# Optimization experiments

Hardware: AMD Instinct MI355X
Metric: run time of the kernel (lower is better)

## Reference

```python
import jax, jax.numpy as jnp
import numpy as np

B, D, S = 16384, 1024, 1024

def _layernorm(x, g, b, eps=1e-5):
    mu = jnp.mean(x, axis=-1, keepdims=True)
    var = jnp.mean(jnp.square(x - mu), axis=-1, keepdims=True)
    return (x - mu) * jax.lax.rsqrt(var + eps) * g + b

def setup_inputs() -> dict:
    key = jax.random.key(0)
    ks = jax.random.split(key, 8)
    inv = lambda n: 1.0 / np.sqrt(n)
    return {
        "x": jax.random.normal(ks[0], (B, D), jnp.float32),
        "s_prev0": jax.random.normal(ks[1], (B, S), jnp.float32),
        "s_prev1": jax.random.normal(ks[2], (B, S), jnp.float32),
        "Wi": jax.random.uniform(ks[3], (4 * S, D), jnp.float32, -inv(D), inv(D)),
        "Ws": jax.random.uniform(ks[4], (4 * S, 2 * S), jnp.float32, -inv(2 * S), inv(2 * S)),
        "lni_g": jnp.ones((4 * S,), jnp.float32),
        "lni_b": jnp.zeros((4 * S,), jnp.float32),
        "lns_g": jnp.ones((4 * S,), jnp.float32),
        "lns_b": jnp.zeros((4 * S,), jnp.float32),
        "lnh_g": jnp.ones((S,), jnp.float32),
        "lnh_b": jnp.zeros((S,), jnp.float32),
    }

def reference(x, s_prev0, s_prev1, Wi, Ws, lni_g, lni_b, lns_g, lns_b, lnh_g, lnh_b):
    s = jnp.concatenate([s_prev0, s_prev1], axis=-1)  # [B, 2S]
    igates = _layernorm(x @ Wi.T, lni_g, lni_b)        # [B, 4S]
    sgates = _layernorm(s @ Ws.T, lns_g, lns_b)        # [B, 4S]
    gates = igates + sgates
    r_inv, i, n, l = jnp.split(gates, 4, axis=1)
    s_n = sgates[:, 2 * S:3 * S]
    l = jax.nn.sigmoid(l)
    r_inv = jax.nn.sigmoid(r_inv)
    i = jax.nn.sigmoid(i)
    n = jnp.tanh(n - r_inv * s_n)
    h = n + i * (l * s_prev0 + (1.0 - l) * s_prev1 - n)
    return _layernorm(h, lnh_g, lnh_b)
```

## Files before the change

### kernel.cpp

```cpp
#include <hip/hip_runtime.h>
#include <cstdint>


typedef unsigned short ushort_t;
typedef __attribute__((ext_vector_type(8))) __bf16 bf16x8;
typedef __attribute__((ext_vector_type(4))) float f32x4;

__device__ __forceinline__ ushort_t f2b(float f) {
    unsigned u = __float_as_uint(f);
    unsigned r = (u + 0x7fffu + ((u >> 16) & 1u)) >> 16;
    return (ushort_t)r;
}
__device__ __forceinline__ float b2f(ushort_t u) {
    return __uint_as_float(((unsigned)u) << 16);
}

__device__ __forceinline__ void gl_lds16(const void* g, void* l) {
    __builtin_amdgcn_global_load_lds(
        (const __attribute__((address_space(1))) unsigned int*)(uintptr_t)g,
        (__attribute__((address_space(3))) unsigned int*)(uintptr_t)l,
        16, 0, 0);
}

#define LOG2E 1.4426950408889634f
__device__ __forceinline__ float fexp2(float x) { return __builtin_amdgcn_exp2f(x); }
__device__ __forceinline__ float frcp(float x)  { return __builtin_amdgcn_rcpf(x); }
__device__ __forceinline__ float fsigmoid(float x) {
    return frcp(1.f + fexp2(-LOG2E * x));
}
__device__ __forceinline__ float ftanh(float y) {
    return 1.f - 2.f * frcp(1.f + fexp2((2.f * LOG2E) * y));
}

__global__ __launch_bounds__(256) void cast_bf16(const float* __restrict__ src,
                                                 ushort_t* __restrict__ dst, long n) {
    long i = ((long)blockIdx.x * 256 + threadIdx.x) * 4;
    if (i + 3 < n) {
        float4 v = *(const float4*)(src + i);
        ushort4 u;
        u.x = f2b(v.x); u.y = f2b(v.y); u.z = f2b(v.z); u.w = f2b(v.w);
        *(ushort4*)(dst + i) = u;
    }
}

__global__ __launch_bounds__(256) void cast_concat(const float* __restrict__ s0,
                                                   const float* __restrict__ s1,
                                                   ushort_t* __restrict__ dst) {
    long i = ((long)blockIdx.x * 256 + threadIdx.x) * 4;
    long row = i >> 11;
    int  col = (int)(i & 2047);
    const float* src = (col < 1024) ? (s0 + row * 1024 + col)
                                    : (s1 + row * 1024 + (col - 1024));
    float4 v = *(const float4*)src;
    ushort4 u;
    u.x = f2b(v.x); u.y = f2b(v.y); u.z = f2b(v.z); u.w = f2b(v.w);
    *(ushort4*)(dst + i) = u;
}


__device__ __forceinline__ void stage2(const char* s0, const char* s1,
                                       int d0, int d1, char* ldsbase,
                                       int kt, int NT) {
    if (kt < NT) {
        long kb = (long)kt << 7;
        char* lb = ldsbase + ((kt & 1) << 15);
        gl_lds16(s0 + kb, lb + d0);
        gl_lds16(s1 + kb, lb + d1);
    }
}

#define SGB_MFMA(n) __builtin_amdgcn_sched_group_barrier(0x8, n, 0)
#define SGB_DSR(n)  __builtin_amdgcn_sched_group_barrier(0x100, n, 0)

#define MFMA_II(Q, II, BS)                                                    \
    _Pragma("unroll") for (int jj = 0; jj < 2; jj++)                          \
        _Pragma("unroll") for (int kh = 0; kh < 2; kh++)                      \
            acc[Q][II][jj] = __builtin_amdgcn_mfma_f32_16x16x32_bf16(         \
                af[II][kh], bfr[BS][jj][kh], acc[Q][II][jj], 0, 0, 0);

#define MFMA_JJ(Q, JJ, BS)                                                    \
    _Pragma("unroll") for (int ii = 0; ii < 4; ii++)                          \
        _Pragma("unroll") for (int kh = 0; kh < 2; kh++)                      \
            acc[Q][ii][JJ] = __builtin_amdgcn_mfma_f32_16x16x32_bf16(         \
                af[ii][kh], bfr[BS][JJ][kh], acc[Q][ii][JJ], 0, 0, 0);

#define RD_B(BASE, R16, KC) (*(const bf16x8*)((BASE) + brow + (R16) * 2048 + (KC)))
#define RD_A(BASE, R16, KC) (*(const bf16x8*)((BASE) + arow + (R16) * 2048 + (KC)))

__global__ __launch_bounds__(512, 2) void gemm_bt(const ushort_t* __restrict__ A,
                                                  const ushort_t* __restrict__ W,
                                                  ushort_t* __restrict__ C,
                                                  int M, int N, int K) {
    (void)M;
    __shared__ __align__(16) ushort_t As[2][256 * 64];
    __shared__ __align__(16) ushort_t Bs[2][256 * 64];

    const int NT   = K >> 6;
    const int t    = threadIdx.x;
    const int lane = t & 63;
    const int w    = t >> 6;
    const int gm   = w >> 2;
    const int gn   = w & 3;
    const int gb   = gn & 1;
    const int wm   = gm << 7;
    const int wn   = gn << 6;

    const int nwg  = gridDim.x;
    const int cpx  = nwg >> 3;
    const int orig = blockIdx.x;
    const int wgid = (orig & 7) * cpx + (orig >> 3);
    const int NXB  = N >> 8;
    const int bx   = wgid % NXB;
    const int by   = wgid / NXB;
    const int bm0  = by << 8;
    const int bn0  = bx << 8;

    const int u0r = t >> 3;
    const int chb = (t & 7) << 4;
    const int cbs = chb ^ ((u0r & 7) << 4);
    const int ur0 = u0r, ur1 = 64 + u0r;

    #define AER(ur) ((ur) < 64 ? (ur) : (ur) + 128)
    #define ALR(ur) ((ur) + 64)
    #define BER(ur) (((((ur) >> 5) >> 1) << 7) + ((((ur) >> 5) & 1) * 96) + ((ur) & 31))
    #define BLR(ur) ((ur) + 32 + (((ur) >> 6) << 6))

    const char* sAe0 = (const char*)(A + (long)(bm0 + AER(ur0)) * K) + cbs;
    const char* sAe1 = (const char*)(A + (long)(bm0 + AER(ur1)) * K) + cbs;
    const char* sAl0 = (const char*)(A + (long)(bm0 + ALR(ur0)) * K) + cbs;
    const char* sAl1 = (const char*)(A + (long)(bm0 + ALR(ur1)) * K) + cbs;
    const char* sBe0 = (const char*)(W + (long)(bn0 + BER(ur0)) * K) + cbs;
    const char* sBe1 = (const char*)(W + (long)(bn0 + BER(ur1)) * K) + cbs;
    const char* sBl0 = (const char*)(W + (long)(bn0 + BLR(ur0)) * K) + cbs;
    const char* sBl1 = (const char*)(W + (long)(bn0 + BLR(ur1)) * K) + cbs;

    const int dAe0 = AER(ur0) * 128 + chb, dAe1 = AER(ur1) * 128 + chb;
    const int dAl0 = ALR(ur0) * 128 + chb, dAl1 = ALR(ur1) * 128 + chb;
    const int dBe0 = BER(ur0) * 128 + chb, dBe1 = BER(ur1) * 128 + chb;
    const int dBl0 = BLR(ur0) * 128 + chb, dBl1 = BLR(ur1) * 128 + chb;

    char* Abase = (char*)&As[0][0];
    char* Bbase = (char*)&Bs[0][0];

    const int ml   = lane & 15;
    const int g    = lane >> 4;
    const int rsw  = (lane & 7) << 4;
    const int kc0  = ((g << 4)) ^ rsw;
    const int kc1  = (64 | (g << 4)) ^ rsw;
    const int arow = (wm + ml) << 7;
    const int brow = (wn + ml) << 7;

    f32x4 acc[4][4][2];
#pragma unroll
    for (int q = 0; q < 4; q++)
#pragma unroll
        for (int ii = 0; ii < 4; ii++)
#pragma unroll
            for (int jj = 0; jj < 2; jj++)
                acc[q][ii][jj] = (f32x4){0.f, 0.f, 0.f, 0.f};

    bf16x8 af[4][2];
    bf16x8 bfr[2][2][2];

    stage2(sAe0, sAe1, dAe0, dAe1, Abase, 0, NT);
    stage2(sAl0, sAl1, dAl0, dAl1, Abase, 0, NT);
    stage2(sBe0, sBe1, dBe0, dBe1, Bbase, 0, NT);
    stage2(sBl0, sBl1, dBl0, dBl1, Bbase, 0, NT);
    stage2(sAe0, sAe1, dAe0, dAe1, Abase, 1, NT);
    stage2(sBe0, sBe1, dBe0, dBe1, Bbase, 1, NT);
    asm volatile("s_waitcnt vmcnt(4)" ::: "memory");
    __builtin_amdgcn_s_barrier();
#pragma unroll
    for (int jj = 0; jj < 2; jj++) {
        bfr[0][jj][0] = RD_B(Bbase, (gb << 1) + jj, kc0);
        bfr[0][jj][1] = RD_B(Bbase, (gb << 1) + jj, kc1);
    }
#pragma unroll
    for (int ii = 0; ii < 4; ii++) {
        af[ii][0] = RD_A(Abase, (gm << 2) + ii, kc0);
        af[ii][1] = RD_A(Abase, (gm << 2) + ii, kc1);
    }

    for (int kt = 0; kt < NT; ++kt) {
        const char* AbT = Abase + ((kt & 1) << 15);
        const char* BbT = Bbase + ((kt & 1) << 15);
        const char* AbN = Abase + (((kt + 1) & 1) << 15);
        const char* BbN = Bbase + (((kt + 1) & 1) << 15);
        const int rB1 = (1 ^ gb) << 1;
        const int rB0 = gb << 1;
        const int rA1 = (1 ^ gm) << 2;
        const int rA0 = gm << 2;

        stage2(sAl0, sAl1, dAl0, dAl1, Abase, kt + 1, NT);
        __builtin_amdgcn_s_barrier();
        __builtin_amdgcn_s_setprio(1);
        MFMA_II(0, 0, 0); SGB_MFMA(4);
        bfr[1][0][0] = RD_B(BbT, rB1 + 0, kc0); SGB_DSR(1);
        MFMA_II(0, 1, 0); SGB_MFMA(4);
        bfr[1][0][1] = RD_B(BbT, rB1 + 0, kc1); SGB_DSR(1);
        MFMA_II(0, 2, 0); SGB_MFMA(4);
        bfr[1][1][0] = RD_B(BbT, rB1 + 1, kc0); SGB_DSR(1);
        MFMA_II(0, 3, 0); SGB_MFMA(4);
        bfr[1][1][1] = RD_B(BbT, rB1 + 1, kc1); SGB_DSR(1);
        __builtin_amdgcn_s_setprio(0);

        stage2(sBl0, sBl1, dBl0, dBl1, Bbase, kt + 1, NT);
        __builtin_amdgcn_s_barrier();
        __builtin_amdgcn_s_setprio(1);
        MFMA_II(1, 0, 1); SGB_MFMA(4);
        af[0][0] = RD_A(AbT, rA1 + 0, kc0);
        af[0][1] = RD_A(AbT, rA1 + 0, kc1); SGB_DSR(2);
        MFMA_II(1, 1, 1); SGB_MFMA(4);
        af[1][0] = RD_A(AbT, rA1 + 1, kc0);
        af[1][1] = RD_A(AbT, rA1 + 1, kc1); SGB_DSR(2);
        MFMA_II(1, 2, 1); SGB_MFMA(4);
        af[2][0] = RD_A(AbT, rA1 + 2, kc0);
        af[2][1] = RD_A(AbT, rA1 + 2, kc1); SGB_DSR(2);
        MFMA_II(1, 3, 1); SGB_MFMA(4);
        af[3][0] = RD_A(AbT, rA1 + 3, kc0);
        af[3][1] = RD_A(AbT, rA1 + 3, kc1); SGB_DSR(2);
        __builtin_amdgcn_s_setprio(0);

        __builtin_amdgcn_s_barrier();
        __builtin_amdgcn_s_setprio(1);
        MFMA_JJ(2, 0, 0);
        MFMA_JJ(2, 1, 0);
        __builtin_amdgcn_s_setprio(0);

        stage2(sAe0, sAe1, dAe0, dAe1, Abase, kt + 2, NT);
        stage2(sBe0, sBe1, dBe0, dBe1, Bbase, kt + 2, NT);
        if (kt < NT - 2) asm volatile("s_waitcnt vmcnt(4)" ::: "memory");
        else             asm volatile("s_waitcnt vmcnt(0)" ::: "memory");
        __builtin_amdgcn_s_barrier();
        __builtin_amdgcn_s_setprio(1);
        MFMA_II(3, 0, 1); SGB_MFMA(4);
        af[0][0] = RD_A(AbN, rA0 + 0, kc0);
        af[0][1] = RD_A(AbN, rA0 + 0, kc1);
        bfr[0][0][0] = RD_B(BbN, rB0 + 0, kc0);
        bfr[0][0][1] = RD_B(BbN, rB0 + 0, kc1); SGB_DSR(4);
        MFMA_II(3, 1, 1); SGB_MFMA(4);
        af[1][0] = RD_A(AbN, rA0 + 1, kc0);
        af[1][1] = RD_A(AbN, rA0 + 1, kc1);
        bfr[0][1][0] = RD_B(BbN, rB0 + 1, kc0);
        bfr[0][1][1] = RD_B(BbN, rB0 + 1, kc1); SGB_DSR(4);
        MFMA_II(3, 2, 1); SGB_MFMA(4);
        af[2][0] = RD_A(AbN, rA0 + 2, kc0);
        af[2][1] = RD_A(AbN, rA0 + 2, kc1); SGB_DSR(2);
        MFMA_II(3, 3, 1); SGB_MFMA(4);
        af[3][0] = RD_A(AbN, rA0 + 3, kc0);
        af[3][1] = RD_A(AbN, rA0 + 3, kc1); SGB_DSR(2);
        __builtin_amdgcn_s_setprio(0);
    }

    const int quad = (lane >> 4) << 2;
#pragma unroll
    for (int q = 0; q < 4; ++q) {
        const int qm = (q >> 1) ^ gm;
        const int qn = (q & 1) ^ gb;
#pragma unroll
        for (int ii = 0; ii < 4; ii++)
#pragma unroll
            for (int jj = 0; jj < 2; jj++)
#pragma unroll
                for (int r = 0; r < 4; r++) {
                    const int cm = bm0 + wm + ((qm << 2) + ii) * 16 + quad + r;
                    const int cn = bn0 + wn + ((qn << 1) + jj) * 16 + ml;
                    C[(long)cm * N + cn] = f2b(acc[q][ii][jj][r]);
                }
    }
}

__global__ __launch_bounds__(256) void fuse_ln(const ushort_t* __restrict__ M1,
                                               const ushort_t* __restrict__ M2,
                                               const float* __restrict__ p0,
                                               const float* __restrict__ p1,
                                               const float* __restrict__ lni_g,
                                               const float* __restrict__ lni_b,
                                               const float* __restrict__ lns_g,
                                               const float* __restrict__ lns_b,
                                               const float* __restrict__ lnh_g,
                                               const float* __restrict__ lnh_b,
                                               float* __restrict__ out) {
    const int row = blockIdx.x;
    const int t   = threadIdx.x;
    const long base = (long)row * 4096;

    __shared__ float sred[16];
    __shared__ float stats[8];

    float v1[4][4], v2[4][4];
    float s1 = 0.f, q1 = 0.f, s2 = 0.f, q2 = 0.f;
#pragma unroll
    for (int q = 0; q < 4; q++) {
        ushort4 a = *(const ushort4*)(M1 + base + q * 1024 + t * 4);
        ushort4 b = *(const ushort4*)(M2 + base + q * 1024 + t * 4);
        const ushort_t* ap = (const ushort_t*)&a;
        const ushort_t* bp = (const ushort_t*)&b;
#pragma unroll
        for (int j = 0; j < 4; j++) {
            float f1 = b2f(ap[j]); v1[q][j] = f1; s1 += f1; q1 += f1 * f1;
            float f2 = b2f(bp[j]); v2[q][j] = f2; s2 += f2; q2 += f2 * f2;
        }
    }
    float r4[4] = {s1, q1, s2, q2};
#pragma unroll
    for (int off = 32; off > 0; off >>= 1) {
#pragma unroll
        for (int i = 0; i < 4; i++) r4[i] += __shfl_down(r4[i], off, 64);
    }
    if ((t & 63) == 0) {
        int w = t >> 6;
#pragma unroll
        for (int i = 0; i < 4; i++) sred[w * 4 + i] = r4[i];
    }
    __syncthreads();
    if (t == 0) {
        float S1 = 0, Q1 = 0, S2 = 0, Q2 = 0;
        for (int w = 0; w < 4; w++) {
            S1 += sred[w * 4]; Q1 += sred[w * 4 + 1];
            S2 += sred[w * 4 + 2]; Q2 += sred[w * 4 + 3];
        }
        float mu1 = S1 * (1.f / 4096.f), mu2 = S2 * (1.f / 4096.f);
        float var1 = Q1 * (1.f / 4096.f) - mu1 * mu1;
        float var2 = Q2 * (1.f / 4096.f) - mu2 * mu2;
        stats[0] = mu1; stats[1] = rsqrtf(var1 + 1e-5f);
        stats[2] = mu2; stats[3] = rsqrtf(var2 + 1e-5f);
    }
    __syncthreads();
    const float mu1 = stats[0], rs1 = stats[1], mu2 = stats[2], rs2 = stats[3];

    float4 Gi[4], Bi[4], Gs[4], Bs[4];
#pragma unroll
    for (int q = 0; q < 4; q++) {
        Gi[q] = *(const float4*)(lni_g + q * 1024 + t * 4);
        Bi[q] = *(const float4*)(lni_b + q * 1024 + t * 4);
        Gs[q] = *(const float4*)(lns_g + q * 1024 + t * 4);
        Bs[q] = *(const float4*)(lns_b + q * 1024 + t * 4);
    }
    float4 P0 = *(const float4*)(p0 + (long)row * 1024 + t * 4);
    float4 P1 = *(const float4*)(p1 + (long)row * 1024 + t * 4);

    float h[4];
    float sh = 0.f, qh = 0.f;
#pragma unroll
    for (int j = 0; j < 4; j++) {
        float gq[4], snv = 0.f;
#pragma unroll
        for (int q = 0; q < 4; q++) {
            float a = (v1[q][j] - mu1) * rs1 * ((const float*)&Gi[q])[j] + ((const float*)&Bi[q])[j];
            float b = (v2[q][j] - mu2) * rs2 * ((const float*)&Gs[q])[j] + ((const float*)&Bs[q])[j];
            if (q == 2) snv = b;
            gq[q] = a + b;
        }
        float rg = fsigmoid(gq[0]);
        float ig = fsigmoid(gq[1]);
        float lg = fsigmoid(gq[3]);
        float ng = ftanh(gq[2] - rg * snv);
        float pp0 = ((const float*)&P0)[j], pp1 = ((const float*)&P1)[j];
        float hv = ng + ig * (lg * pp0 + (1.f - lg) * pp1 - ng);
        h[j] = hv; sh += hv; qh += hv * hv;
    }
    float r2[2] = {sh, qh};
#pragma unroll
    for (int off = 32; off > 0; off >>= 1) {
#pragma unroll
        for (int i = 0; i < 2; i++) r2[i] += __shfl_down(r2[i], off, 64);
    }
    if ((t & 63) == 0) {
        int w = t >> 6;
        sred[w * 4] = r2[0]; sred[w * 4 + 1] = r2[1];
    }
    __syncthreads();
    if (t == 0) {
        float S = 0, Q = 0;
        for (int w = 0; w < 4; w++) { S += sred[w * 4]; Q += sred[w * 4 + 1]; }
        float mu = S * (1.f / 1024.f);
        float var = Q * (1.f / 1024.f) - mu * mu;
        stats[4] = mu; stats[5] = rsqrtf(var + 1e-5f);
    }
    __syncthreads();
    const float muh = stats[4], rsh = stats[5];

    float4 Gh = *(const float4*)(lnh_g + t * 4);
    float4 Bh = *(const float4*)(lnh_b + t * 4);
    float4 O;
#pragma unroll
    for (int j = 0; j < 4; j++)
        ((float*)&O)[j] = (h[j] - muh) * rsh * ((const float*)&Gh)[j] + ((const float*)&Bh)[j];
    *(float4*)(out + (long)row * 1024 + t * 4) = O;
}

extern "C" void kernel_launch(void* const* d_in, const int* in_sizes, int n_in,
                              void* d_out, int out_size, void* d_ws, size_t ws_size,
                              hipStream_t stream) {
    const float* x     = (const float*)d_in[0];
    const float* s0    = (const float*)d_in[1];
    const float* s1    = (const float*)d_in[2];
    const float* Wi    = (const float*)d_in[3];
    const float* Ws    = (const float*)d_in[4];
    const float* lni_g = (const float*)d_in[5];
    const float* lni_b = (const float*)d_in[6];
    const float* lns_g = (const float*)d_in[7];
    const float* lns_b = (const float*)d_in[8];
    const float* lnh_g = (const float*)d_in[9];
    const float* lnh_b = (const float*)d_in[10];
    float* out = (float*)d_out;

    char* wsb = (char*)d_ws;
    ushort_t* M1  = (ushort_t*)wsb;
    ushort_t* M2  = (ushort_t*)(wsb + (((size_t)128) << 20));
    ushort_t* Wsb = (ushort_t*)wsb;
    ushort_t* sb  = (ushort_t*)d_out;
    ushort_t* xb  = (ushort_t*)d_out;
    ushort_t* Wib = (ushort_t*)((char*)d_out + (((size_t)32) << 20));

    dim3 g(1024);

    cast_concat<<<32768, 256, 0, stream>>>(s0, s1, sb);
    cast_bf16<<<8192, 256, 0, stream>>>(Ws, Wsb, (long)4096 * 2048);
    gemm_bt<<<g, 512, 0, stream>>>(sb, Wsb, M2, 16384, 4096, 2048);
    cast_bf16<<<16384, 256, 0, stream>>>(x, xb, (long)16384 * 1024);
    cast_bf16<<<4096, 256, 0, stream>>>(Wi, Wib, (long)4096 * 1024);
    gemm_bt<<<g, 512, 0, stream>>>(xb, Wib, M1, 16384, 4096, 1024);
    fuse_ln<<<16384, 256, 0, stream>>>(M1, M2, s0, s1, lni_g, lni_b, lns_g,
                                       lns_b, lnh_g, lnh_b, out);
}
```

Measured before the change: 743.2 us.

## Process fused LayerNorm rows per wavefront with shuffle-only reductions

The fused gate/LayerNorm epilogue now assigns whole rows to single wavefronts, each handling two rows, in place of one row per 256-thread block. Reductions become butterfly xor shuffles within the wave, which removes the shared-memory exchange and the four __syncthreads per row. Each lane processes 16 contiguous columns with 16-byte loads. The cost is more registers per lane and scalar per-element loads of the gamma/beta vectors, which may raise register pressure and lower occupancy.

```diff
diff --git a/kernel.cpp b/kernel.cpp
--- a/kernel.cpp
+++ b/kernel.cpp
@@ -270,6 +270,7 @@
     }
 }
 
+#define FL_RPW 2
 __global__ __launch_bounds__(256) void fuse_ln(const ushort_t* __restrict__ M1,
                                                const ushort_t* __restrict__ M2,
                                                const float* __restrict__ p0,
@@ -281,113 +282,109 @@
                                                const float* __restrict__ lnh_g,
                                                const float* __restrict__ lnh_b,
                                                float* __restrict__ out) {
-    const int row = blockIdx.x;
-    const int t   = threadIdx.x;
-    const long base = (long)row * 4096;
-
-    __shared__ float sred[16];
-    __shared__ float stats[8];
-
-    float v1[4][4], v2[4][4];
-    float s1 = 0.f, q1 = 0.f, s2 = 0.f, q2 = 0.f;
-#pragma unroll
-    for (int q = 0; q < 4; q++) {
-        ushort4 a = *(const ushort4*)(M1 + base + q * 1024 + t * 4);
-        ushort4 b = *(const ushort4*)(M2 + base + q * 1024 + t * 4);
-        const ushort_t* ap = (const ushort_t*)&a;
-        const ushort_t* bp = (const ushort_t*)&b;
-#pragma unroll
-        for (int j = 0; j < 4; j++) {
-            float f1 = b2f(ap[j]); v1[q][j] = f1; s1 += f1; q1 += f1 * f1;
-            float f2 = b2f(bp[j]); v2[q][j] = f2; s2 += f2; q2 += f2 * f2;
+    const int lane = threadIdx.x & 63;
+    const int wv   = threadIdx.x >> 6;
+    const int wave = blockIdx.x * 4 + wv;
+    const int col0 = lane << 4;
+
+    for (int r = 0; r < FL_RPW; ++r) {
+        const int row = wave * FL_RPW + r;
+        const long gbase = (long)row * 4096;
+        const long pbase = (long)row * 1024 + col0;
+
+        uint4 a[4][2], b[4][2];
+#pragma unroll
+        for (int q = 0; q < 4; q++)
+#pragma unroll
+            for (int h2 = 0; h2 < 2; h2++) {
+                a[q][h2] = *(const uint4*)(M1 + gbase + q * 1024 + col0 + h2 * 8);
+                b[q][h2] = *(const uint4*)(M2 + gbase + q * 1024 + col0 + h2 * 8);
+            }
+        float4 P0v[4], P1v[4];
+#pragma unroll
+        for (int c = 0; c < 4; c++) {
+            P0v[c] = *(const float4*)(p0 + pbase + c * 4);
+            P1v[c] = *(const float4*)(p1 + pbase + c * 4);
         }
-    }
-    float r4[4] = {s1, q1, s2, q2};
-#pragma unroll
-    for (int off = 32; off > 0; off >>= 1) {
-#pragma unroll
-        for (int i = 0; i < 4; i++) r4[i] += __shfl_down(r4[i], off, 64);
-    }
-    if ((t & 63) == 0) {
-        int w = t >> 6;
-#pragma unroll
-        for (int i = 0; i < 4; i++) sred[w * 4 + i] = r4[i];
-    }
-    __syncthreads();
-    if (t == 0) {
-        float S1 = 0, Q1 = 0, S2 = 0, Q2 = 0;
-        for (int w = 0; w < 4; w++) {
-            S1 += sred[w * 4]; Q1 += sred[w * 4 + 1];
-            S2 += sred[w * 4 + 2]; Q2 += sred[w * 4 + 3];
+
+        float s1 = 0.f, q1 = 0.f, s2 = 0.f, q2 = 0.f;
+#pragma unroll
+        for (int q = 0; q < 4; q++)
+#pragma unroll
+            for (int h2 = 0; h2 < 2; h2++)
+#pragma unroll
+                for (int u = 0; u < 4; u++) {
+                    unsigned ua = ((const unsigned*)&a[q][h2])[u];
+                    unsigned ub = ((const unsigned*)&b[q][h2])[u];
+                    float f;
+                    f = __uint_as_float(ua << 16);          s1 += f; q1 += f * f;
+                    f = __uint_as_float(ua & 0xffff0000u);  s1 += f; q1 += f * f;
+                    f = __uint_as_float(ub << 16);          s2 += f; q2 += f * f;
+                    f = __uint_as_float(ub & 0xffff0000u);  s2 += f; q2 += f * f;
+                }
+        float rr[4] = {s1, q1, s2, q2};
+#pragma unroll
+        for (int off = 1; off < 64; off <<= 1)
+#pragma unroll
+            for (int i = 0; i < 4; i++) rr[i] += __shfl_xor(rr[i], off, 64);
+        const float mu1 = rr[0] * (1.f / 4096.f), mu2 = rr[2] * (1.f / 4096.f);
+        const float rs1 = rsqrtf(rr[1] * (1.f / 4096.f) - mu1 * mu1 + 1e-5f);
+        const float rs2 = rsqrtf(rr[3] * (1.f / 4096.f) - mu2 * mu2 + 1e-5f);
+
+        float h[16];
+        float sh = 0.f, qh = 0.f;
+#pragma unroll
+        for (int c = 0; c < 4; c++) {
+#pragma unroll
+            for (int jl = 0; jl < 4; jl++) {
+                const int j = c * 4 + jl;
+                float gq[4], snv = 0.f;
+#pragma unroll
+                for (int q = 0; q < 4; q++) {
+                    const float gi = lni_g[q * 1024 + col0 + j];
+                    const float bi = lni_b[q * 1024 + col0 + j];
+                    const float gs = lns_g[q * 1024 + col0 + j];
+                    const float bs = lns_b[q * 1024 + col0 + j];
+                    unsigned ua = ((const unsigned*)&a[q][j >> 3])[(j >> 1) & 3];
+                    unsigned ub = ((const unsigned*)&b[q][j >> 3])[(j >> 1) & 3];
+                    float f1 = (j & 1) ? __uint_as_float(ua & 0xffff0000u)
+                                       : __uint_as_float(ua << 16);
+                    float f2 = (j & 1) ? __uint_as_float(ub & 0xffff0000u)
+                                       : __uint_as_float(ub << 16);
+                    float av = (f1 - mu1) * rs1 * gi + bi;
+                    float bv = (f2 - mu2) * rs2 * gs + bs;
+                    if (q == 2) snv = bv;
+                    gq[q] = av + bv;
+                }
+                float rg = fsigmoid(gq[0]);
+                float ig = fsigmoid(gq[1]);
+                float lg = fsigmoid(gq[3]);
+                float ng = ftanh(gq[2] - rg * snv);
+                float pp0 = ((const float*)&P0v[c])[jl], pp1 = ((const float*)&P1v[c])[jl];
+                float hv = ng + ig * (lg * pp0 + (1.f - lg) * pp1 - ng);
+                h[j] = hv; sh += hv; qh += hv * hv;
+            }
         }
-        float mu1 = S1 * (1.f / 4096.f), mu2 = S2 * (1.f / 4096.f);
-        float var1 = Q1 * (1.f / 4096.f) - mu1 * mu1;
-        float var2 = Q2 * (1.f / 4096.f) - mu2 * mu2;
-        stats[0] = mu1; stats[1] = rsqrtf(var1 + 1e-5f);
-        stats[2] = mu2; stats[3] = rsqrtf(var2 + 1e-5f);
-    }
-    __syncthreads();
-    const float mu1 = stats[0], rs1 = stats[1], mu2 = stats[2], rs2 = stats[3];
-
-    float4 Gi[4], Bi[4], Gs[4], Bs[4];
-#pragma unroll
-    for (int q = 0; q < 4; q++) {
-        Gi[q] = *(const float4*)(lni_g + q * 1024 + t * 4);
-        Bi[q] = *(const float4*)(lni_b + q * 1024 + t * 4);
-        Gs[q] = *(const float4*)(lns_g + q * 1024 + t * 4);
-        Bs[q] = *(const float4*)(lns_b + q * 1024 + t * 4);
-    }
-    float4 P0 = *(const float4*)(p0 + (long)row * 1024 + t * 4);
-    float4 P1 = *(const float4*)(p1 + (long)row * 1024 + t * 4);
-
-    float h[4];
-    float sh = 0.f, qh = 0.f;
-#pragma unroll
-    for (int j = 0; j < 4; j++) {
-        float gq[4], snv = 0.f;
-#pragma unroll
-        for (int q = 0; q < 4; q++) {
-            float a = (v1[q][j] - mu1) * rs1 * ((const float*)&Gi[q])[j] + ((const float*)&Bi[q])[j];
-            float b = (v2[q][j] - mu2) * rs2 * ((const float*)&Gs[q])[j] + ((const float*)&Bs[q])[j];
-            if (q == 2) snv = b;
-            gq[q] = a + b;
+        float r2[2] = {sh, qh};
+#pragma unroll
+        for (int off = 1; off < 64; off <<= 1)
+#pragma unroll
+            for (int i = 0; i < 2; i++) r2[i] += __shfl_xor(r2[i], off, 64);
+        const float muh = r2[0] * (1.f / 1024.f);
+        const float rsh = rsqrtf(r2[1] * (1.f / 1024.f) - muh * muh + 1e-5f);
+
+#pragma unroll
+        for (int c = 0; c < 4; c++) {
+            float4 Gh4 = *(const float4*)(lnh_g + col0 + c * 4);
+            float4 Bh4 = *(const float4*)(lnh_b + col0 + c * 4);
+            float4 O;
+#pragma unroll
+            for (int jl = 0; jl < 4; jl++)
+                ((float*)&O)[jl] = (h[c * 4 + jl] - muh) * rsh *
+                                   ((const float*)&Gh4)[jl] + ((const float*)&Bh4)[jl];
+            *(float4*)(out + pbase + c * 4) = O;
         }
-        float rg = fsigmoid(gq[0]);
-        float ig = fsigmoid(gq[1]);
-        float lg = fsigmoid(gq[3]);
-        float ng = ftanh(gq[2] - rg * snv);
-        float pp0 = ((const float*)&P0)[j], pp1 = ((const float*)&P1)[j];
-        float hv = ng + ig * (lg * pp0 + (1.f - lg) * pp1 - ng);
-        h[j] = hv; sh += hv; qh += hv * hv;
-    }
-    float r2[2] = {sh, qh};
-#pragma unroll
-    for (int off = 32; off > 0; off >>= 1) {
-#pragma unroll
-        for (int i = 0; i < 2; i++) r2[i] += __shfl_down(r2[i], off, 64);
-    }
-    if ((t & 63) == 0) {
-        int w = t >> 6;
-        sred[w * 4] = r2[0]; sred[w * 4 + 1] = r2[1];
-    }
-    __syncthreads();
-    if (t == 0) {
-        float S = 0, Q = 0;
-        for (int w = 0; w < 4; w++) { S += sred[w * 4]; Q += sred[w * 4 + 1]; }
-        float mu = S * (1.f / 1024.f);
-        float var = Q * (1.f / 1024.f) - mu * mu;
-        stats[4] = mu; stats[5] = rsqrtf(var + 1e-5f);
-    }
-    __syncthreads();
-    const float muh = stats[4], rsh = stats[5];
-
-    float4 Gh = *(const float4*)(lnh_g + t * 4);
-    float4 Bh = *(const float4*)(lnh_b + t * 4);
-    float4 O;
-#pragma unroll
-    for (int j = 0; j < 4; j++)
-        ((float*)&O)[j] = (h[j] - muh) * rsh * ((const float*)&Gh)[j] + ((const float*)&Bh)[j];
-    *(float4*)(out + (long)row * 1024 + t * 4) = O;
+    }
 }
 
 extern "C" void kernel_launch(void* const* d_in, const int* in_sizes, int n_in,
@@ -422,6 +419,7 @@
     cast_bf16<<<16384, 256, 0, stream>>>(x, xb, (long)16384 * 1024);
     cast_bf16<<<4096, 256, 0, stream>>>(Wi, Wib, (long)4096 * 1024);
     gemm_bt<<<g, 512, 0, stream>>>(xb, Wib, M1, 16384, 4096, 1024);
-    fuse_ln<<<16384, 256, 0, stream>>>(M1, M2, s0, s1, lni_g, lni_b, lns_g,
-                                       lns_b, lnh_g, lnh_b, out);
-}
+    fuse_ln<<<16384 / (4 * FL_RPW), 256, 0, stream>>>(M1, M2, s0, s1, lni_g,
+                                                      lni_b, lns_g, lns_b,
+                                                      lnh_g, lnh_b, out);
+}
```

Measured after the change: 814.4 us. +9.6%, slower.
